# Kernel tuning notes

Hardware: AMD Instinct MI355X
Metric: run time of the kernel (lower is better)

Reference implementation:

```python
import jax, jax.numpy as jnp
import numpy as np

B, L, D, H = 2, 2048, 1024, 16
HD = D // H
ROPE_BASE = 10000.0


def _chain_info(lengths):
    """lengths: [B, L] int, chain lengths packed at the front, zeros after.
    Returns per-position within-chain positions (RoPE resets per chain),
    chain ids, and a validity mask."""
    def one(row):
        csum = jnp.cumsum(row)                      # [L]
        total = csum[-1]
        p = jnp.arange(L)
        cid = jnp.searchsorted(csum, p, side='right')  # chain id per position
        prev = jnp.where(cid > 0, csum[jnp.clip(cid - 1, 0, L - 1)], 0)
        valid = p < total
        pos = jnp.where(valid, p - prev, 0).astype(jnp.float32)
        return pos, cid, valid
    return jax.vmap(one)(lengths)


def _rope_tables(pos):
    # pos: [B, L] float -> cos/sin [B, L, 1, HD]
    inv_freq = 1.0 / (ROPE_BASE ** (jnp.arange(0, HD, 2, dtype=jnp.float32) / HD))
    freqs = pos[..., None] * inv_freq               # [B, L, HD/2]
    emb = jnp.concatenate([freqs, freqs], axis=-1)  # [B, L, HD]
    return jnp.cos(emb)[:, :, None, :], jnp.sin(emb)[:, :, None, :]


def _apply_rope(x, cos, sin):
    d = x.shape[-1]
    x1, x2 = x[..., : d // 2], x[..., d // 2:]
    return x * cos + jnp.concatenate([-x2, x1], axis=-1) * sin


def _branch(x, Wqkv, bqkv, cos, sin, allowed):
    # x: [B, L, D]; allowed: [B, L, L] bool attention mask for this branch
    qkv = x @ Wqkv.T + bqkv                          # [B, L, 3D]
    qkv = qkv.reshape(B, L, 3, H, HD)
    q, k, v = qkv[:, :, 0], qkv[:, :, 1], qkv[:, :, 2]
    q = q * (HD ** -0.5)
    q = _apply_rope(q, cos, sin)
    k = _apply_rope(k, cos, sin)
    scores = jnp.einsum('bthd,bshd->bhts', q, k)     # [B, H, L, L]
    scores = jnp.where(allowed[:, None], scores, -jnp.inf)
    probs = jax.nn.softmax(scores, axis=-1)
    probs = jnp.where(jnp.isnan(probs), 0.0, probs)  # fully-masked rows -> 0
    out = jnp.einsum('bhts,bshd->bthd', probs, v)    # [B, L, H, HD]
    return out.reshape(B, L, D)


def setup_inputs() -> dict:
    key = jax.random.key(0)
    ks = jax.random.split(key, 7)
    s = 0.02
    lens = np.zeros((B, L), np.int64)
    lens[0, :8] = [300, 250, 200, 400, 350, 248, 150, 100]   # sum 1998
    lens[1, :6] = [512, 400, 300, 360, 276, 200]             # sum 2048
    return {
        'hidden_states': jax.random.normal(ks[0], (B, L, D), jnp.float32),
        'attention_mask_in_length': jnp.asarray(lens),
        'Wqkv_intra': jax.random.normal(ks[1], (3 * D, D), jnp.float32) * s,
        'bqkv_intra': jnp.zeros((3 * D,), jnp.float32),
        'Wqkv_inter': jax.random.normal(ks[2], (3 * D, D), jnp.float32) * s,
        'bqkv_inter': jnp.zeros((3 * D,), jnp.float32),
        'Wout': jax.random.normal(ks[3], (D, D), jnp.float32) * s,
        'bout': jnp.zeros((D,), jnp.float32),
    }


def reference(hidden_states, attention_mask_in_length, Wqkv_intra, bqkv_intra,
              Wqkv_inter, bqkv_inter, Wout, bout):
    pos, cid, valid = _chain_info(attention_mask_in_length)
    cos, sin = _rope_tables(pos)
    same_chain = cid[:, :, None] == cid[:, None, :]          # [B, L, L]
    key_valid = valid[:, None, :]                            # [B, 1, L]
    allowed_intra = same_chain & key_valid
    allowed_inter = (~same_chain) & key_valid
    out_intra = _branch(hidden_states, Wqkv_intra, bqkv_intra, cos, sin, allowed_intra)
    out_inter = _branch(hidden_states, Wqkv_inter, bqkv_inter, cos, sin, allowed_inter)
    return (out_intra + out_inter) @ Wout.T + bout
```

## Files before the change

kernel.cpp:

```cpp
#include <hip/hip_runtime.h>
#include <hip/hip_bf16.h>
#include <stdint.h>

#define B 2
#define L 2048
#define D 1024
#define H 16
#define HD 64
#define NT (L / 64)
#define NQT2 (L / 256)
#define INVALID_CID 0x40000000
#define BHLHD ((size_t)B * H * L * HD)

typedef __hip_bfloat16 bf16;
typedef __attribute__((ext_vector_type(8))) short short8;
typedef __attribute__((ext_vector_type(4))) float floatx4;
typedef __attribute__((ext_vector_type(4))) unsigned int uint4v;

static __device__ __forceinline__ short f2bf(float f) {
    bf16 h = __float2bfloat16(f);
    return *reinterpret_cast<short*>(&h);
}

static __device__ __forceinline__ void async_copy16(const void* g, void* l) {
    __builtin_amdgcn_global_load_lds((__attribute__((address_space(1))) void*)g,
                                     (__attribute__((address_space(3))) void*)l,
                                     16, 0, 0);
}

__global__ void chain_kernel(const int* __restrict__ lens,
                             float* __restrict__ pos, int* __restrict__ cid,
                             int4* __restrict__ tinfo)
{
    __shared__ int csum[L];
    __shared__ int cids[L];
    __shared__ int part[256];
    int b = blockIdx.x;
    int t = threadIdx.x;

    int loc[8];
    int s = 0;
    #pragma unroll
    for (int j = 0; j < 8; ++j) { s += lens[b * L + t * 8 + j]; loc[j] = s; }
    part[t] = s;
    __syncthreads();

    #pragma unroll
    for (int d = 1; d < 256; d <<= 1) {
        int v = (t >= d) ? part[t - d] : 0;
        __syncthreads();
        part[t] += v;
        __syncthreads();
    }
    int base = (t > 0) ? part[t - 1] : 0;
    #pragma unroll
    for (int j = 0; j < 8; ++j) csum[t * 8 + j] = base + loc[j];
    __syncthreads();

    int total = csum[L - 1];
    for (int p = t; p < L; p += 256) {
        int cv;
        if (p < total) {
            int lo = 0, hi = L;
            while (lo < hi) {
                int mid = (lo + hi) >> 1;
                if (csum[mid] <= p) lo = mid + 1; else hi = mid;
            }
            int prev = (lo > 0) ? csum[lo - 1] : 0;
            pos[b * L + p] = (float)(p - prev);
            cv = lo;
        } else {
            pos[b * L + p] = 0.f;
            cv = INVALID_CID;
        }
        cids[p] = cv;
        cid[b * L + p] = cv;
    }
    __syncthreads();
    if (t < NT) {
        int mn = 0x7fffffff, mx = -1, any = 0, all = 1;
        for (int j = 0; j < 64; ++j) {
            int cv = cids[t * 64 + j];
            if (cv != INVALID_CID) { any = 1; mn = min(mn, cv); mx = max(mx, cv); }
            else all = 0;
        }
        tinfo[b * NT + t] = make_int4(mn, mx, any | (all << 1), 0);
    }
}

__global__ void prep_kernel(const float* __restrict__ x,  const float* __restrict__ Wi,
                            const float* __restrict__ We, const float* __restrict__ Wo,
                            bf16* __restrict__ xb, bf16* __restrict__ Wib,
                            bf16* __restrict__ Web, bf16* __restrict__ Wob,
                            const float* __restrict__ pos, float2* __restrict__ tab)
{
    int bid = blockIdx.x;
    if (bid < 11264) {
        const float* src; bf16* dst; int base;
        if      (bid < 4096)  { src = x;  dst = xb;  base = bid; }
        else if (bid < 7168)  { src = Wi; dst = Wib; base = bid - 4096; }
        else if (bid < 10240) { src = We; dst = Web; base = bid - 7168; }
        else                  { src = Wo; dst = Wob; base = bid - 10240; }
        int i = (base * 256 + threadIdx.x) * 4;
        float4 v = *(const float4*)(src + i);
        dst[i + 0] = __float2bfloat16(v.x);
        dst[i + 1] = __float2bfloat16(v.y);
        dst[i + 2] = __float2bfloat16(v.z);
        dst[i + 3] = __float2bfloat16(v.w);
    } else {
        int idx = (bid - 11264) * 256 + threadIdx.x;
        int j = idx & 31, l = idx >> 5;
        float invf = exp2f(-(float)j * (13.287712379549449f / 32.f));
        float ang = pos[l] * invf;
        tab[idx] = make_float2(cosf(ang), sinf(ang));
    }
}

__global__ __launch_bounds__(256, 4) void gemm_qkv(
    const bf16* __restrict__ A, const bf16* __restrict__ Bw,
    const float* __restrict__ bi, const float* __restrict__ be,
    const float2* __restrict__ tab,
    bf16* __restrict__ Qo, bf16* __restrict__ Ko, bf16* __restrict__ Vto)
{
    __shared__ short Smem[4 * 128 * 32];

    int tid = threadIdx.x;
    int wave = tid >> 6, lane = tid & 63;
    int i15 = lane & 15, q8 = lane >> 4;
    int wm = wave & 1, wn = wave >> 1;
    int m0 = blockIdx.y * 128, n0 = blockIdx.x * 128;
    const int K = D;

    floatx4 acc[4][4];
    #pragma unroll
    for (int mt = 0; mt < 4; ++mt)
        #pragma unroll
        for (int nt = 0; nt < 4; ++nt) acc[mt][nt] = (floatx4){0.f, 0.f, 0.f, 0.f};

    const short* gA = (const short*)A  + (size_t)(m0 + wave * 32 + (lane >> 2)) * K + (lane & 3) * 8;
    const short* gB = (const short*)Bw + (size_t)(n0 + wave * 32 + (lane >> 2)) * K + (lane & 3) * 8;

    auto stage = [&](int bufp, int kt) {
        short* lA = Smem + bufp * 8192 + wave * 1024;
        short* lB = lA + 4096;
        async_copy16(gA + kt,          lA);
        async_copy16(gA + 16 * K + kt, lA + 512);
        async_copy16(gB + kt,          lB);
        async_copy16(gB + 16 * K + kt, lB + 512);
    };

    stage(0, 0);
    __syncthreads();

    int cur = 0;
    for (int kt = 0; kt < K; kt += 32) {
        if (kt + 32 < K) stage(cur ^ 1, kt + 32);

        const short* As = Smem + cur * 8192;
        const short* Bs = As + 4096;
        short8 af[4], bfr[4];
        #pragma unroll
        for (int mt = 0; mt < 4; ++mt)
            af[mt] = *(const short8*)&As[(wm * 64 + mt * 16 + i15) * 32 + q8 * 8];
        #pragma unroll
        for (int nt = 0; nt < 4; ++nt)
            bfr[nt] = *(const short8*)&Bs[(wn * 64 + nt * 16 + i15) * 32 + q8 * 8];
        #pragma unroll
        for (int mt = 0; mt < 4; ++mt)
            #pragma unroll
            for (int nt = 0; nt < 4; ++nt)
                acc[mt][nt] = __builtin_amdgcn_mfma_f32_16x16x32_bf16(af[mt], bfr[nt], acc[mt][nt], 0, 0, 0);

        __syncthreads();
        cur ^= 1;
    }

    int nb = n0 + wn * 64;
    int segw = nb >> 10;
    int br = (segw >= 3);
    int st = segw - 3 * br;
    int h = (nb >> 6) & (H - 1);
    int b = m0 >> 11;
    int lb = (m0 & (L - 1)) + wm * 64;

    float bv[4];
    #pragma unroll
    for (int nt = 0; nt < 4; ++nt) {
        int n = nb + nt * 16 + i15;
        bv[nt] = (n < 3 * D) ? bi[n] : be[n - 3 * D];
    }

    if (st != 2) {
        bf16* out = (st == 0 ? Qo : Ko) + (size_t)br * BHLHD;
        const size_t bh = (size_t)(b * H + h) * L;
        float qs = (st == 0) ? 0.18033688011111772f : 1.0f;
        #pragma unroll
        for (int mt = 0; mt < 4; ++mt) {
            #pragma unroll
            for (int rg = 0; rg < 4; ++rg) {
                int m = m0 + wm * 64 + mt * 16 + q8 * 4 + rg;
                int l = lb + mt * 16 + q8 * 4 + rg;
                float2 cs0 = tab[(size_t)m * 32 + i15];
                float2 cs1 = tab[(size_t)m * 32 + 16 + i15];
                size_t orow = (bh + l) * HD;
                #pragma unroll
                for (int nt = 0; nt < 4; ++nt) {
                    float x  = acc[mt][nt][rg] + bv[nt];
                    float pr = acc[mt][nt ^ 2][rg] + bv[nt ^ 2];
                    float cc = (nt & 1) ? cs1.x : cs0.x;
                    float ss = (nt & 1) ? cs1.y : cs0.y;
                    float v = qs * (x * cc + ((nt < 2) ? -pr : pr) * ss);
                    out[orow + nt * 16 + i15] = __float2bfloat16(v);
                }
            }
        }
    } else {
        bf16* out = Vto + (size_t)br * BHLHD;
        const size_t bhd = (size_t)(b * H + h) * HD;
        __syncthreads();
        short* vts = Smem + wave * 64 * 20;
        #pragma unroll
        for (int mt = 0; mt < 4; ++mt) {
            #pragma unroll
            for (int nt = 0; nt < 4; ++nt) {
                uint2 w;
                w.x = (unsigned)(unsigned short)f2bf(acc[mt][nt][0] + bv[nt]) |
                      ((unsigned)(unsigned short)f2bf(acc[mt][nt][1] + bv[nt]) << 16);
                w.y = (unsigned)(unsigned short)f2bf(acc[mt][nt][2] + bv[nt]) |
                      ((unsigned)(unsigned short)f2bf(acc[mt][nt][3] + bv[nt]) << 16);
                *(uint2*)&vts[(nt * 16 + i15) * 20 + q8 * 4] = w;
            }
            uint2 r0 = *(const uint2*)&vts[lane * 20 + 0];
            uint2 r1 = *(const uint2*)&vts[lane * 20 + 4];
            uint2 r2 = *(const uint2*)&vts[lane * 20 + 8];
            uint2 r3 = *(const uint2*)&vts[lane * 20 + 12];
            size_t ga = (bhd + lane) * L + lb + mt * 16;
            uint4v v0 = (uint4v){r0.x, r0.y, r1.x, r1.y};
            uint4v v1 = (uint4v){r2.x, r2.y, r3.x, r3.y};
            *(uint4v*)&out[ga]     = v0;
            *(uint4v*)&out[ga + 8] = v1;
        }
    }
}

__global__ __launch_bounds__(256, 4) void gemm128(
    const bf16* __restrict__ A, const bf16* __restrict__ Bw,
    const float* __restrict__ bias, void* __restrict__ Cout,
    int M, int N, int K, int c_bf16)
{
    __shared__ short Smem[4 * 128 * 32];

    int tid = threadIdx.x;
    int wave = tid >> 6, lane = tid & 63;
    int i15 = lane & 15, q8 = lane >> 4;
    int wm = wave & 1, wn = wave >> 1;
    int m0 = blockIdx.y * 128, n0 = blockIdx.x * 128;

    floatx4 acc[4][4];
    #pragma unroll
    for (int mt = 0; mt < 4; ++mt)
        #pragma unroll
        for (int nt = 0; nt < 4; ++nt) acc[mt][nt] = (floatx4){0.f, 0.f, 0.f, 0.f};

    const short* gA = (const short*)A  + (size_t)(m0 + wave * 32 + (lane >> 2)) * K + (lane & 3) * 8;
    const short* gB = (const short*)Bw + (size_t)(n0 + wave * 32 + (lane >> 2)) * K + (lane & 3) * 8;

    auto stage = [&](int bufp, int kt) {
        short* lA = Smem + bufp * 8192 + wave * 1024;
        short* lB = lA + 4096;
        async_copy16(gA + kt,          lA);
        async_copy16(gA + 16 * K + kt, lA + 512);
        async_copy16(gB + kt,          lB);
        async_copy16(gB + 16 * K + kt, lB + 512);
    };

    stage(0, 0);
    __syncthreads();

    int cur = 0;
    for (int kt = 0; kt < K; kt += 32) {
        if (kt + 32 < K) stage(cur ^ 1, kt + 32);

        const short* As = Smem + cur * 8192;
        const short* Bs = As + 4096;
        short8 af[4], bfr[4];
        #pragma unroll
        for (int mt = 0; mt < 4; ++mt)
            af[mt] = *(const short8*)&As[(wm * 64 + mt * 16 + i15) * 32 + q8 * 8];
        #pragma unroll
        for (int nt = 0; nt < 4; ++nt)
            bfr[nt] = *(const short8*)&Bs[(wn * 64 + nt * 16 + i15) * 32 + q8 * 8];
        #pragma unroll
        for (int mt = 0; mt < 4; ++mt)
            #pragma unroll
            for (int nt = 0; nt < 4; ++nt)
                acc[mt][nt] = __builtin_amdgcn_mfma_f32_16x16x32_bf16(af[mt], bfr[nt], acc[mt][nt], 0, 0, 0);

        __syncthreads();
        cur ^= 1;
    }

    #pragma unroll
    for (int nt = 0; nt < 4; ++nt) {
        int n = n0 + wn * 64 + nt * 16 + i15;
        float bv = bias[n];
        #pragma unroll
        for (int mt = 0; mt < 4; ++mt) {
            #pragma unroll
            for (int rg = 0; rg < 4; ++rg) {
                int m = m0 + wm * 64 + mt * 16 + q8 * 4 + rg;
                float v = acc[mt][nt][rg] + bv;
                if (c_bf16) ((bf16*)Cout)[(size_t)m * N + n] = __float2bfloat16(v);
                else        ((float*)Cout)[(size_t)m * N + n] = v;
            }
        }
    }
}

__global__ __launch_bounds__(512, 2) void attn11(
    const bf16* __restrict__ Qg, const bf16* __restrict__ Kgg, const bf16* __restrict__ Vtgg,
    const int* __restrict__ cid, const int4* __restrict__ tinfo,
    bf16* __restrict__ Out)
{
    __shared__ short Ks[2][64][72];
    __shared__ short Vs[2][64][72];
    __shared__ int cls0_s[NT], cls1_s[NT];
    __shared__ int list_s[2][NT];
    __shared__ int nlist_s[2];

    int tid = threadIdx.x;
    int wave = tid >> 6, lane = tid & 63;
    int i15 = lane & 15, q8 = lane >> 4;
    int workid = ((blockIdx.x & 7) << 5) | (blockIdx.x >> 3);
    int qt = workid & (NQT2 - 1);
    int h  = (workid >> 3) & (H - 1);
    int b  = workid >> 7;
    int q0 = qt * 256;
    const size_t bh  = (size_t)(b * H + h) * L;
    const size_t bhd = (size_t)(b * H + h) * HD;

    int cq[2];
    #pragma unroll
    for (int g = 0; g < 2; ++g)
        cq[g] = cid[b * L + q0 + g * 128 + wave * 16 + i15];

    int4 qinf;
    {
        int4 e0 = tinfo[b * NT + 4 * qt];
        int4 e1 = tinfo[b * NT + 4 * qt + 1];
        int4 e2 = tinfo[b * NT + 4 * qt + 2];
        int4 e3 = tinfo[b * NT + 4 * qt + 3];
        qinf.x = min(min(e0.x, e1.x), min(e2.x, e3.x));
        qinf.y = max(max(e0.y, e1.y), max(e2.y, e3.y));
        qinf.z = ((e0.z | e1.z | e2.z | e3.z) & 1) | (e0.z & e1.z & e2.z & e3.z & 2);
    }
    int qall = (qinf.z >> 1) & 1;

    if (tid < NT) {
        int4 ki = tinfo[b * NT + tid];
        int kany = ki.z & 1, kall = (ki.z >> 1) & 1;
        bool disjoint = (ki.x > qinf.y) || (ki.y < qinf.x);
        bool mono = qall && kall && (qinf.x == qinf.y) && (ki.x == ki.y) && (qinf.x == ki.x);
        cls0_s[tid] = (!kany || disjoint) ? 0 : (mono ? 2 : 1);
        cls1_s[tid] = (!kany || mono) ? 0 : ((kall && disjoint) ? 2 : 1);
    }
    __syncthreads();
    if (tid < 2) {
        const int* cls = tid ? cls1_s : cls0_s;
        int n = 0;
        for (int t = 0; t < NT; ++t) {
            int c = cls[t];
            if (c) list_s[tid][n++] = (t * 64) | ((c == 2) << 16);
        }
        nlist_s[tid] = n;
    }
    __syncthreads();

    int r = tid >> 3, c8 = (tid & 7) * 8;
    int sr = ((((r >> 2) & 1) | ((r >> 5) << 1)) << 4) | (((r >> 3) & 3) << 2) | (r & 3);

    floatx4 accO[2][2][4];
    #pragma unroll
    for (int br = 0; br < 2; ++br)
        #pragma unroll
        for (int g = 0; g < 2; ++g)
            #pragma unroll
            for (int t = 0; t < 4; ++t) accO[br][g][t] = (floatx4){0.f, 0.f, 0.f, 0.f};
    float lsum[2][2] = {{0.f, 0.f}, {0.f, 0.f}};

    #pragma unroll
    for (int br = 0; br < 2; ++br) {
        const short* Qb    = (const short*)Qg   + (size_t)br * BHLHD;
        const short* Kbase = (const short*)Kgg  + (size_t)br * BHLHD + (bh + r) * HD + c8;
        const short* Vbase = (const short*)Vtgg + (size_t)br * BHLHD + (bhd + r) * L + c8;
        int n = nlist_s[br];

        short8 qf[2][2];
        #pragma unroll
        for (int g = 0; g < 2; ++g) {
            const short* qp = Qb + (bh + q0 + g * 128 + wave * 16 + i15) * HD + q8 * 8;
            qf[g][0] = *(const short8*)(qp);
            qf[g][1] = *(const short8*)(qp + 32);
        }

        int4 pk, pv;
        int cur = 0;
        if (n > 0) {
            cur = list_s[br][0];
            int kt0 = cur & 0xffff;
            pk = *(const int4*)(Kbase + (size_t)kt0 * HD);
            pv = *(const int4*)(Vbase + kt0);
        }
        __syncthreads();

        for (int i = 0; i < n; ++i) {
            int kt = cur & 0xffff, full = cur >> 16;
            int buf = i & 1;

            *(int4*)&Ks[buf][sr][c8] = pk;
            *(int4*)&Vs[buf][r][c8]  = pv;
            __syncthreads();

            if (i + 1 < n) {
                cur = list_s[br][i + 1];
                int nk = cur & 0xffff;
                pk = *(const int4*)(Kbase + (size_t)nk * HD);
                pv = *(const int4*)(Vbase + nk);
            }

            unsigned int dl[2][4], dh[2][4];
            #pragma unroll
            for (int t = 0; t < 4; ++t) {
                short8 b0 = *(const short8*)&Ks[buf][t * 16 + i15][q8 * 8];
                short8 b1 = *(const short8*)&Ks[buf][t * 16 + i15][32 + q8 * 8];

                floatx4 accS[2];
                #pragma unroll
                for (int g = 0; g < 2; ++g) {
                    accS[g] = (floatx4){0.f, 0.f, 0.f, 0.f};
                    accS[g] = __builtin_amdgcn_mfma_f32_16x16x32_bf16(b0, qf[g][0], accS[g], 0, 0, 0);
                    accS[g] = __builtin_amdgcn_mfma_f32_16x16x32_bf16(b1, qf[g][1], accS[g], 0, 0, 0);
                }

                if (!full) {
                    int4 ck4 = *(const int4*)(cid + b * L + kt + (q8 << 3) + ((t & 1) << 2) + ((t >> 1) << 5));
                    int ckr[4] = {ck4.x, ck4.y, ck4.z, ck4.w};
                    #pragma unroll
                    for (int g = 0; g < 2; ++g)
                        #pragma unroll
                        for (int rg = 0; rg < 4; ++rg) {
                            bool kv = (ckr[rg] != INVALID_CID);
                            bool match = (cq[g] == ckr[rg]);
                            bool ok = kv && (br ? !match : match);
                            accS[g][rg] = ok ? accS[g][rg] : -1e30f;
                        }
                }

                #pragma unroll
                for (int g = 0; g < 2; ++g) {
                    float p0 = __builtin_amdgcn_exp2f(accS[g][0]);
                    float p1 = __builtin_amdgcn_exp2f(accS[g][1]);
                    float p2 = __builtin_amdgcn_exp2f(accS[g][2]);
                    float p3 = __builtin_amdgcn_exp2f(accS[g][3]);
                    lsum[br][g] += (p0 + p1) + (p2 + p3);
                    dl[g][t] = (unsigned)(unsigned short)f2bf(p0) | ((unsigned)(unsigned short)f2bf(p1) << 16);
                    dh[g][t] = (unsigned)(unsigned short)f2bf(p2) | ((unsigned)(unsigned short)f2bf(p3) << 16);
                }
            }

            union { uint4v u; short8 s; } pa0[2], pa1[2];
            #pragma unroll
            for (int g = 0; g < 2; ++g) {
                pa0[g].u = (uint4v){dl[g][0], dh[g][0], dl[g][1], dh[g][1]};
                pa1[g].u = (uint4v){dl[g][2], dh[g][2], dl[g][3], dh[g][3]};
            }

            #pragma unroll
            for (int dt = 0; dt < 4; ++dt) {
                short8 vf0 = *(const short8*)&Vs[buf][dt * 16 + i15][q8 * 8];
                short8 vf1 = *(const short8*)&Vs[buf][dt * 16 + i15][32 + q8 * 8];
                #pragma unroll
                for (int g = 0; g < 2; ++g) {
                    accO[br][g][dt] = __builtin_amdgcn_mfma_f32_16x16x32_bf16(pa0[g].s, vf0, accO[br][g][dt], 0, 0, 0);
                    accO[br][g][dt] = __builtin_amdgcn_mfma_f32_16x16x32_bf16(pa1[g].s, vf1, accO[br][g][dt], 0, 0, 0);
                }
            }
        }
    }

    float inv[2][2][4];
    #pragma unroll
    for (int br = 0; br < 2; ++br)
        #pragma unroll
        for (int g = 0; g < 2; ++g) {
            float ls = lsum[br][g];
            ls += __shfl_xor(ls, 16, 64);
            ls += __shfl_xor(ls, 32, 64);
            #pragma unroll
            for (int rg = 0; rg < 4; ++rg) {
                float lv = __shfl(ls, q8 * 4 + rg, 64);
                inv[br][g][rg] = (lv > 0.f) ? 1.f / lv : 0.f;
            }
        }

    #pragma unroll
    for (int g = 0; g < 2; ++g)
        #pragma unroll
        for (int t = 0; t < 4; ++t)
            #pragma unroll
            for (int rg = 0; rg < 4; ++rg) {
                size_t idx = (size_t)(b * L + q0 + g * 128 + wave * 16 + q8 * 4 + rg) * D + h * HD + t * 16 + i15;
                float o = accO[0][g][t][rg] * inv[0][g][rg] + accO[1][g][t][rg] * inv[1][g][rg];
                Out[idx] = __float2bfloat16(o);
            }
}

extern "C" void kernel_launch(void* const* d_in, const int* in_sizes, int n_in,
                              void* d_out, int out_size, void* d_ws, size_t ws_size,
                              hipStream_t stream)
{
    const float* x    = (const float*)d_in[0];
    const int*   mlen = (const int*)  d_in[1];
    const float* Wi   = (const float*)d_in[2];
    const float* bi   = (const float*)d_in[3];
    const float* We   = (const float*)d_in[4];
    const float* be   = (const float*)d_in[5];
    const float* Wo   = (const float*)d_in[6];
    const float* bo   = (const float*)d_in[7];

    char* ws = (char*)d_ws;
    size_t off = 0;
    auto alloc = [&](size_t bytes) {
        void* p = ws + off;
        off += (bytes + 255) & ~(size_t)255;
        return p;
    };
    bf16*  x_b   = (bf16*) alloc((size_t)B * L * D * 2);
    bf16*  Wi_b  = (bf16*) alloc((size_t)3 * D * D * 2);
    bf16*  We_b  = (bf16*) alloc((size_t)3 * D * D * 2);
    bf16*  Wo_b  = (bf16*) alloc((size_t)D * D * 2);
    bf16*  q_b   = (bf16*) alloc(2 * BHLHD * 2);
    bf16*  k_b   = (bf16*) alloc(2 * BHLHD * 2);
    bf16*  vt_b  = (bf16*) alloc(2 * BHLHD * 2);
    bf16*  sum_b = (bf16*) alloc((size_t)B * L * D * 2);
    float* pos   = (float*)alloc((size_t)B * L * 4);
    int*   cid   = (int*)  alloc((size_t)B * L * 4);
    int4*  tinfo = (int4*) alloc((size_t)B * NT * 16);
    float2* rtab = (float2*)alloc((size_t)B * L * 32 * 8);
    (void)ws_size; (void)n_in; (void)in_sizes; (void)out_size;

    chain_kernel<<<B, 256, 0, stream>>>(mlen, pos, cid, tinfo);

    prep_kernel<<<11776, 256, 0, stream>>>(x, Wi, We, Wo, x_b, Wi_b, We_b, Wo_b, pos, rtab);

    dim3 gq(6 * D / 128, B * L / 128);
    gemm_qkv<<<gq, 256, 0, stream>>>(x_b, Wi_b, bi, be, rtab, q_b, k_b, vt_b);

    attn11<<<B * H * NQT2, 512, 0, stream>>>(q_b, k_b, vt_b, cid, tinfo, sum_b);

    dim3 go(D / 128, B * L / 128);
    gemm128<<<go, 256, 0, stream>>>(sum_b, Wo_b, bo, d_out, B * L, D, D, 0);
}
```

Baseline: 279.7 us.

## Load K fragments directly into registers with two-tile prefetch in attention

The attention kernel stops staging K tiles through shared memory. Each wave now loads its K MFMA fragments and chain-id masks straight from global memory into registers, and two tiles (A/B) are kept in flight so the next loads overlap the current tile's compute. Only V still goes through a double-buffered shared-memory slot. Launch bounds drop from 2 to 1 block per CU to leave room for the larger register footprint, which lowers occupancy and adds redundant global K reads across waves.

New measurement: 352.5 us. 26.0% more time.

```diff
diff --git a/kernel.cpp b/kernel.cpp
--- a/kernel.cpp
+++ b/kernel.cpp
@@ -317,12 +317,11 @@
     }
 }
 
-__global__ __launch_bounds__(512, 2) void attn11(
+__global__ __launch_bounds__(512, 1) void attn14(
     const bf16* __restrict__ Qg, const bf16* __restrict__ Kgg, const bf16* __restrict__ Vtgg,
     const int* __restrict__ cid, const int4* __restrict__ tinfo,
     bf16* __restrict__ Out)
 {
-    __shared__ short Ks[2][64][72];
     __shared__ short Vs[2][64][72];
     __shared__ int cls0_s[NT], cls1_s[NT];
     __shared__ int list_s[2][NT];
@@ -377,22 +376,81 @@
     __syncthreads();
 
     int r = tid >> 3, c8 = (tid & 7) * 8;
-    int sr = ((((r >> 2) & 1) | ((r >> 5) << 1)) << 4) | (((r >> 3) & 3) << 2) | (r & 3);
+    int kbase = (i15 & 3) + 8 * (i15 >> 2);
 
     floatx4 accO[2][2][4];
     #pragma unroll
-    for (int br = 0; br < 2; ++br)
+    for (int brq = 0; brq < 2; ++brq)
         #pragma unroll
         for (int g = 0; g < 2; ++g)
             #pragma unroll
-            for (int t = 0; t < 4; ++t) accO[br][g][t] = (floatx4){0.f, 0.f, 0.f, 0.f};
+            for (int t = 0; t < 4; ++t) accO[brq][g][t] = (floatx4){0.f, 0.f, 0.f, 0.f};
     float lsum[2][2] = {{0.f, 0.f}, {0.f, 0.f}};
 
+    auto compute_tile = [&](const short8 (&kf)[4][2], const int4 (&ck)[4], int full,
+                            const short (*Vt)[72], const short8 (&qfb)[2][2],
+                            floatx4 (&aO)[2][4], float (&ls)[2], int brv) {
+        unsigned int dl[2][4], dh[2][4];
+        #pragma unroll
+        for (int t = 0; t < 4; ++t) {
+            floatx4 accS[2];
+            #pragma unroll
+            for (int g = 0; g < 2; ++g) {
+                accS[g] = (floatx4){0.f, 0.f, 0.f, 0.f};
+                accS[g] = __builtin_amdgcn_mfma_f32_16x16x32_bf16(kf[t][0], qfb[g][0], accS[g], 0, 0, 0);
+                accS[g] = __builtin_amdgcn_mfma_f32_16x16x32_bf16(kf[t][1], qfb[g][1], accS[g], 0, 0, 0);
+            }
+
+            if (!full) {
+                int ckr[4] = {ck[t].x, ck[t].y, ck[t].z, ck[t].w};
+                #pragma unroll
+                for (int g = 0; g < 2; ++g)
+                    #pragma unroll
+                    for (int rg = 0; rg < 4; ++rg) {
+                        bool kv = (ckr[rg] != INVALID_CID);
+                        bool match = (cq[g] == ckr[rg]);
+                        bool ok = kv && (brv ? !match : match);
+                        accS[g][rg] = ok ? accS[g][rg] : -1e30f;
+                    }
+            }
+
+            #pragma unroll
+            for (int g = 0; g < 2; ++g) {
+                float p0 = __builtin_amdgcn_exp2f(accS[g][0]);
+                float p1 = __builtin_amdgcn_exp2f(accS[g][1]);
+                float p2 = __builtin_amdgcn_exp2f(accS[g][2]);
+                float p3 = __builtin_amdgcn_exp2f(accS[g][3]);
+                ls[g] += (p0 + p1) + (p2 + p3);
+                dl[g][t] = (unsigned)(unsigned short)f2bf(p0) | ((unsigned)(unsigned short)f2bf(p1) << 16);
+                dh[g][t] = (unsigned)(unsigned short)f2bf(p2) | ((unsigned)(unsigned short)f2bf(p3) << 16);
+            }
+        }
+
+        union { uint4v u; short8 s; } pa0[2], pa1[2];
+        #pragma unroll
+        for (int g = 0; g < 2; ++g) {
+            pa0[g].u = (uint4v){dl[g][0], dh[g][0], dl[g][1], dh[g][1]};
+            pa1[g].u = (uint4v){dl[g][2], dh[g][2], dl[g][3], dh[g][3]};
+        }
+
+        #pragma unroll
+        for (int dt = 0; dt < 4; ++dt) {
+            short8 vf0 = *(const short8*)&Vt[dt * 16 + i15][q8 * 8];
+            short8 vf1 = *(const short8*)&Vt[dt * 16 + i15][32 + q8 * 8];
+            #pragma unroll
+            for (int g = 0; g < 2; ++g) {
+                aO[g][dt] = __builtin_amdgcn_mfma_f32_16x16x32_bf16(pa0[g].s, vf0, aO[g][dt], 0, 0, 0);
+                aO[g][dt] = __builtin_amdgcn_mfma_f32_16x16x32_bf16(pa1[g].s, vf1, aO[g][dt], 0, 0, 0);
+            }
+        }
+    };
+
     #pragma unroll
     for (int br = 0; br < 2; ++br) {
-        const short* Qb    = (const short*)Qg   + (size_t)br * BHLHD;
-        const short* Kbase = (const short*)Kgg  + (size_t)br * BHLHD + (bh + r) * HD + c8;
+        const short* Qb = (const short*)Qg  + (size_t)br * BHLHD;
+        const short* Kw = (const short*)Kgg + (size_t)br * BHLHD + (bh + kbase) * HD + q8 * 8;
         const short* Vbase = (const short*)Vtgg + (size_t)br * BHLHD + (bhd + r) * L + c8;
+        const int*   cb = cid + b * L + (q8 << 3);
         int n = nlist_s[br];
 
         short8 qf[2][2];
@@ -403,86 +461,62 @@
             qf[g][1] = *(const short8*)(qp + 32);
         }
 
-        int4 pk, pv;
-        int cur = 0;
+        auto load_kf = [&](short8 (&kf)[4][2], int kt) {
+            #pragma unroll
+            for (int t = 0; t < 4; ++t) {
+                const short* p = Kw + (size_t)(kt + (t & 1) * 4 + (t >> 1) * 32) * HD;
+                kf[t][0] = *(const short8*)(p);
+                kf[t][1] = *(const short8*)(p + 32);
+            }
+        };
+        auto load_ck = [&](int4 (&ck)[4], int kt) {
+            #pragma unroll
+            for (int t = 0; t < 4; ++t)
+                ck[t] = *(const int4*)(cb + kt + ((t & 1) << 2) + ((t >> 1) << 5));
+        };
+
+        int eA = 0, eB = 0;
+        short8 kfA[4][2], kfB[4][2];
+        int4 ckA[4], ckB[4];
+        int4 pvA, pvB;
         if (n > 0) {
-            cur = list_s[br][0];
-            int kt0 = cur & 0xffff;
-            pk = *(const int4*)(Kbase + (size_t)kt0 * HD);
-            pv = *(const int4*)(Vbase + kt0);
+            eA = list_s[br][0];
+            int kt0 = eA & 0xffff;
+            load_kf(kfA, kt0);
+            load_ck(ckA, kt0);
+            pvA = *(const int4*)(Vbase + kt0);
+        }
+        if (n > 1) {
+            eB = list_s[br][1];
+            int kt1 = eB & 0xffff;
+            load_kf(kfB, kt1);
+            load_ck(ckB, kt1);
+            pvB = *(const int4*)(Vbase + kt1);
         }
         __syncthreads();
 
-        for (int i = 0; i < n; ++i) {
-            int kt = cur & 0xffff, full = cur >> 16;
-            int buf = i & 1;
-
-            *(int4*)&Ks[buf][sr][c8] = pk;
-            *(int4*)&Vs[buf][r][c8]  = pv;
+        for (int i = 0; i < n; i += 2) {
+            *(int4*)&Vs[0][r][c8] = pvA;
             __syncthreads();
+            if (i + 2 < n) pvA = *(const int4*)(Vbase + (list_s[br][i + 2] & 0xffff));
+            compute_tile(kfA, ckA, eA >> 16, Vs[0], qf, accO[br], lsum[br], br);
+            if (i + 2 < n) {
+                eA = list_s[br][i + 2];
+                int nk = eA & 0xffff;
+                load_kf(kfA, nk);
+                load_ck(ckA, nk);
+            }
 
             if (i + 1 < n) {
-                cur = list_s[br][i + 1];
-                int nk = cur & 0xffff;
-                pk = *(const int4*)(Kbase + (size_t)nk * HD);
-                pv = *(const int4*)(Vbase + nk);
-            }
-
-            unsigned int dl[2][4], dh[2][4];
-            #pragma unroll
-            for (int t = 0; t < 4; ++t) {
-                short8 b0 = *(const short8*)&Ks[buf][t * 16 + i15][q8 * 8];
-                short8 b1 = *(const short8*)&Ks[buf][t * 16 + i15][32 + q8 * 8];
-
-                floatx4 accS[2];
-                #pragma unroll
-                for (int g = 0; g < 2; ++g) {
-                    accS[g] = (floatx4){0.f, 0.f, 0.f, 0.f};
-                    accS[g] = __builtin_amdgcn_mfma_f32_16x16x32_bf16(b0, qf[g][0], accS[g], 0, 0, 0);
-                    accS[g] = __builtin_amdgcn_mfma_f32_16x16x32_bf16(b1, qf[g][1], accS[g], 0, 0, 0);
-                }
-
-                if (!full) {
-                    int4 ck4 = *(const int4*)(cid + b * L + kt + (q8 << 3) + ((t & 1) << 2) + ((t >> 1) << 5));
-                    int ckr[4] = {ck4.x, ck4.y, ck4.z, ck4.w};
-                    #pragma unroll
-                    for (int g = 0; g < 2; ++g)
-                        #pragma unroll
-                        for (int rg = 0; rg < 4; ++rg) {
-                            bool kv = (ckr[rg] != INVALID_CID);
-                            bool match = (cq[g] == ckr[rg]);
-                            bool ok = kv && (br ? !match : match);
-                            accS[g][rg] = ok ? accS[g][rg] : -1e30f;
-                        }
-                }
-
-                #pragma unroll
-                for (int g = 0; g < 2; ++g) {
-                    float p0 = __builtin_amdgcn_exp2f(accS[g][0]);
-                    float p1 = __builtin_amdgcn_exp2f(accS[g][1]);
-                    float p2 = __builtin_amdgcn_exp2f(accS[g][2]);
-                    float p3 = __builtin_amdgcn_exp2f(accS[g][3]);
-                    lsum[br][g] += (p0 + p1) + (p2 + p3);
-                    dl[g][t] = (unsigned)(unsigned short)f2bf(p0) | ((unsigned)(unsigned short)f2bf(p1) << 16);
-                    dh[g][t] = (unsigned)(unsigned short)f2bf(p2) | ((unsigned)(unsigned short)f2bf(p3) << 16);
-                }
-            }
-
-            union { uint4v u; short8 s; } pa0[2], pa1[2];
-            #pragma unroll
-            for (int g = 0; g < 2; ++g) {
-                pa0[g].u = (uint4v){dl[g][0], dh[g][0], dl[g][1], dh[g][1]};
-                pa1[g].u = (uint4v){dl[g][2], dh[g][2], dl[g][3], dh[g][3]};
-            }
-
-            #pragma unroll
-            for (int dt = 0; dt < 4; ++dt) {
-                short8 vf0 = *(const short8*)&Vs[buf][dt * 16 + i15][q8 * 8];
-                short8 vf1 = *(const short8*)&Vs[buf][dt * 16 + i15][32 + q8 * 8];
-                #pragma unroll
-                for (int g = 0; g < 2; ++g) {
-                    accO[br][g][dt] = __builtin_amdgcn_mfma_f32_16x16x32_bf16(pa0[g].s, vf0, accO[br][g][dt], 0, 0, 0);
-                    accO[br][g][dt] = __builtin_amdgcn_mfma_f32_16x16x32_bf16(pa1[g].s, vf1, accO[br][g][dt], 0, 0, 0);
+                *(int4*)&Vs[1][r][c8] = pvB;
+                __syncthreads();
+                if (i + 3 < n) pvB = *(const int4*)(Vbase + (list_s[br][i + 3] & 0xffff));
+                compute_tile(kfB, ckB, eB >> 16, Vs[1], qf, accO[br], lsum[br], br);
+                if (i + 3 < n) {
+                    eB = list_s[br][i + 3];
+                    int nk = eB & 0xffff;
+                    load_kf(kfB, nk);
+                    load_ck(ckB, nk);
                 }
             }
         }
@@ -556,7 +590,7 @@
     dim3 gq(6 * D / 128, B * L / 128);
     gemm_qkv<<<gq, 256, 0, stream>>>(x_b, Wi_b, bi, be, rtab, q_b, k_b, vt_b);
 
-    attn11<<<B * H * NQT2, 512, 0, stream>>>(q_b, k_b, vt_b, cid, tinfo, sum_b);
+    attn14<<<B * H * NQT2, 512, 0, stream>>>(q_b, k_b, vt_b, cid, tinfo, sum_b);
 
     dim3 go(D / 128, B * L / 128);
     gemm128<<<go, 256, 0, stream>>>(sum_b, Wo_b, bo, d_out, B * L, D, D, 0);
```
